# Performance work log

Measured on AMD Instinct MI355X. Metric: run time of the kernel, lower is better.

## Reference

```python
import jax, jax.numpy as jnp
import numpy as np

N_NODES = 100000
N_EDGES = 1600000
IN_C, HID_C, OUT_C = 128, 128, 64


def setup_inputs() -> dict:
    key = jax.random.key(0)
    ks = jax.random.split(key, 8)
    x = jax.random.normal(ks[0], (N_NODES, IN_C), dtype=jnp.float32)
    edge_index = jax.random.randint(ks[1], (2, N_EDGES), 0, N_NODES, dtype=jnp.int32)
    # Glorot-ish init for GCNConv linear weights, zero bias (PyG default)
    def glorot(k, fan_in, fan_out):
        s = jnp.sqrt(6.0 / (fan_in + fan_out))
        return jax.random.uniform(k, (fan_in, fan_out), dtype=jnp.float32, minval=-s, maxval=s)
    return {
        "x": x,
        "edge_index": edge_index,
        "W1": glorot(ks[2], IN_C, HID_C), "b1": jnp.zeros((HID_C,), jnp.float32),
        "W2": glorot(ks[3], HID_C, HID_C), "b2": jnp.zeros((HID_C,), jnp.float32),
        "W3": glorot(ks[4], HID_C, OUT_C), "b3": jnp.zeros((OUT_C,), jnp.float32),
    }


def _gcn_norm(edge_index, num_nodes):
    # Add self-loops (PyG GCNConv default) and compute symmetric normalization
    loops = jnp.arange(num_nodes, dtype=edge_index.dtype)
    src = jnp.concatenate([edge_index[0], loops])  # [E+N]
    dst = jnp.concatenate([edge_index[1], loops])
    deg = jax.ops.segment_sum(jnp.ones_like(dst, dtype=jnp.float32), dst,
                              num_segments=num_nodes)
    deg_inv_sqrt = jnp.where(deg > 0, jax.lax.rsqrt(jnp.maximum(deg, 1.0)), 0.0)
    norm = deg_inv_sqrt[src] * deg_inv_sqrt[dst]  # [E+N]
    return src, dst, norm


def _gcn_layer(x, src, dst, norm, W, b, num_nodes):
    h = x @ W                                # [N, out] dense transform first
    msg = h[src] * norm[:, None]             # gather + scale  [E+N, out]
    out = jax.ops.segment_sum(msg, dst, num_segments=num_nodes)  # scatter-add
    return out + b


def reference(x, edge_index, W1, b1, W2, b2, W3, b3):
    n = x.shape[0]
    src, dst, norm = _gcn_norm(edge_index, n)
    h = jax.nn.relu(_gcn_layer(x, src, dst, norm, W1, b1, n))
    h = jax.nn.relu(_gcn_layer(h, src, dst, norm, W2, b2, n))
    return _gcn_layer(h, src, dst, norm, W3, b3, n)
```

## Files before the change

### kernel.cpp

```cpp
#include <hip/hip_runtime.h>

#define NN 100000
#define NE 1600000
#define NBK 391
#define BSH 8
#define MPAD 100096
#define SCB 391
#define CAP 5120
#define NB64 1563

typedef unsigned short ushortT;
typedef unsigned long long ull;
using sh8 = __attribute__((ext_vector_type(8))) short;
using f4  = __attribute__((ext_vector_type(4))) float;


__device__ __forceinline__ unsigned short bfr(float f) {
  unsigned u = __float_as_uint(f);
  u += 0x7FFF + ((u >> 16) & 1);
  return (unsigned short)(u >> 16);
}
__device__ __forceinline__ float bf2f(unsigned short h) {
  return __uint_as_float(((unsigned)h) << 16);
}
__device__ __forceinline__ void acc8(const uint4 v, float* a) {
  a[0] += __uint_as_float(v.x << 16);
  a[1] += __uint_as_float(v.x & 0xFFFF0000u);
  a[2] += __uint_as_float(v.y << 16);
  a[3] += __uint_as_float(v.y & 0xFFFF0000u);
  a[4] += __uint_as_float(v.z << 16);
  a[5] += __uint_as_float(v.z & 0xFFFF0000u);
  a[6] += __uint_as_float(v.w << 16);
  a[7] += __uint_as_float(v.w & 0xFFFF0000u);
}
__device__ __forceinline__ sh8 hi8(const float4 a, const float4 b) {
  sh8 r;
  r[0] = (short)bfr(a.x); r[1] = (short)bfr(a.y);
  r[2] = (short)bfr(a.z); r[3] = (short)bfr(a.w);
  r[4] = (short)bfr(b.x); r[5] = (short)bfr(b.y);
  r[6] = (short)bfr(b.z); r[7] = (short)bfr(b.w);
  return r;
}


template <int COUT>
__device__ __forceinline__ void packone(const float* __restrict__ W,
                                        ushortT* __restrict__ Bp, int i) {
  const int j = i & 7;
  const int l = (i >> 3) & 63;
  const int rest = i >> 9;
  const int g = rest % (COUT / 16);
  const int ks = rest / (COUT / 16);
  const int k = (ks & 3) * 32 + (l >> 4) * 8 + j;
  const int n = g * 16 + (l & 15);
  const float v = W[k * COUT + n];
  const unsigned short h = bfr(v);
  Bp[i] = (ks < 4) ? h : bfr(v - bf2f(h));
}


__global__ __launch_bounds__(256) void k_scatterpack(
    const int* __restrict__ src, const int* __restrict__ dst,
    int* __restrict__ cursor, unsigned* __restrict__ pairArr,
    const float* __restrict__ W1, const float* __restrict__ W2,
    const float* __restrict__ W3, ushortT* __restrict__ Bp1,
    ushortT* __restrict__ Bp2, ushortT* __restrict__ Bp3) {
  if (blockIdx.x >= SCB) {
    const int i = (blockIdx.x - SCB) * 256 + threadIdx.x;
    if (i < 32768) packone<128>(W1, Bp1, i);
    else if (i < 65536) packone<128>(W2, Bp2, i - 32768);
    else packone<64>(W3, Bp3, i - 65536);
    return;
  }
  __shared__ int lcnt[512];
  __shared__ int lbase[512];
  __shared__ int lrank[NBK];
  __shared__ int bbase[NBK];
  __shared__ int sd2[256];
  __shared__ unsigned sorted[4096];
  __shared__ int target[4096];
  const int t = threadIdx.x;
  for (int i = t; i < 512; i += 256) lcnt[i] = 0;
  for (int i = t; i < NBK; i += 256) lrank[i] = 0;
  __syncthreads();
  const int base = blockIdx.x * 4096;
  int rs[16], rd[16];
#pragma unroll
  for (int q = 0; q < 16; q++) {
    int e = base + t + 256 * q;
    rs[q] = (e < NE) ? src[e] : -1;
    rd[q] = (e < NE) ? dst[e] : -1;
    if (rd[q] >= 0) atomicAdd(&lcnt[rd[q] >> BSH], 1);
  }
  __syncthreads();
  const int s0 = lcnt[2 * t];
  const int s1 = lcnt[2 * t + 1];
  sd2[t] = s0 + s1;
  __syncthreads();
  for (int off = 1; off < 256; off <<= 1) {
    int x = (t >= off) ? sd2[t - off] : 0;
    __syncthreads();
    sd2[t] += x;
    __syncthreads();
  }
  const int epair = sd2[t] - (s0 + s1);
  lbase[2 * t] = epair;
  lbase[2 * t + 1] = epair + s0;
  __syncthreads();
  for (int i = t; i < NBK; i += 256)
    if (lcnt[i] > 0) bbase[i] = atomicAdd(&cursor[i], lcnt[i]);
  __syncthreads();
#pragma unroll
  for (int q = 0; q < 16; q++) {
    if (rd[q] >= 0) {
      int b = rd[q] >> BSH;
      int r = atomicAdd(&lrank[b], 1);
      int slot = lbase[b] + r;
      sorted[slot] = ((unsigned)rs[q] << 8) | ((unsigned)rd[q] & 255u);
      target[slot] = b * CAP + bbase[b] + r;
    }
  }
  __syncthreads();
  const int n = min(4096, NE - base);
  for (int s = t; s < n; s += 256) pairArr[target[s]] = sorted[s];
}


__global__ __launch_bounds__(256) void k_buildcsr(const unsigned* __restrict__ pairArr,
                                                  const int* __restrict__ cnt,
                                                  float* __restrict__ dinv,
                                                  int* __restrict__ rowptr,
                                                  int* __restrict__ col) {
  __shared__ int lc[256];
  __shared__ int sd[256];
  __shared__ int bc[NBK];
  const int t = threadIdx.x;
  const int b = blockIdx.x;
  const int n0 = b << BSH;
  for (int i = t; i < NBK; i += 256) bc[i] = cnt[i];
  lc[t] = 0;
  __syncthreads();
  int partial = 0;
  for (int i = t; i < b; i += 256) partial += bc[i];
  sd[t] = partial;
  __syncthreads();
  for (int off = 128; off > 0; off >>= 1) {
    if (t < off) sd[t] += sd[t + off];
    __syncthreads();
  }
  const int ebeg = sd[0];
  const int myCnt = bc[b];
  __syncthreads();
  const unsigned* pb = pairArr + (size_t)b * CAP;
  for (int i = t; i < myCnt; i += 256)
    atomicAdd(&lc[pb[i] & 255u], 1);
  __syncthreads();
  const int v = lc[t];
  sd[t] = v;
  __syncthreads();
  for (int off = 1; off < 256; off <<= 1) {
    int x = (t >= off) ? sd[t - off] : 0;
    __syncthreads();
    sd[t] += x;
    __syncthreads();
  }
  const int excl = sd[t] - v;
  lc[t] = excl;
  const int node = n0 + t;
  if (node < NN) {
    rowptr[node] = ebeg + excl;
    dinv[node] = rsqrtf(1.0f + (float)v);
  }
  if (b == 0 && t == 0) rowptr[NN] = NE;
  __syncthreads();
  for (int i = t; i < myCnt; i += 256) {
    unsigned p = pb[i];
    int d = (int)(p & 255u);
    int srcv = (int)(p >> 8);
    int pos = atomicAdd(&lc[d], 1);
    col[ebeg + pos] = srcv;
  }
}


template <int COUT, bool FUSED>
__global__ __launch_bounds__(256) void k_gemmM(const ushortT* __restrict__ A,
                                               const float* __restrict__ X,
                                               const ushortT* __restrict__ Bp,
                                               const float* __restrict__ dinv,
                                               ushortT* __restrict__ hs) {
  constexpr int CGALL = COUT / 16;
  constexpr int RG = 2;
  constexpr int CG = 4;
  const int w = threadIdx.x >> 6;
  const int lane = threadIdx.x & 63;
  const int q = lane >> 4;
  const int c = lane & 15;
  int row0, cg0;
  if (COUT == 128) {
    row0 = blockIdx.x * 64 + (w & 1) * 32;
    cg0 = (w >> 1) * 4;
  } else {
    row0 = blockIdx.x * 128 + w * 32;
    cg0 = 0;
  }

  const ushortT* ap[RG];
  const float* xp[RG];
#pragma unroll
  for (int rg = 0; rg < RG; rg++) {
    const int row = row0 + rg * 16 + c;
    if (FUSED) xp[rg] = X + (size_t)min(row, NN - 1) * 128 + q * 8;
    else ap[rg] = A + (size_t)row * 128 + q * 8;
  }
  const ushortT* bp0 = Bp + (size_t)lane * 8;

  f4 acc[RG][CG];
#pragma unroll
  for (int i = 0; i < RG; i++)
#pragma unroll
    for (int j = 0; j < CG; j++) acc[i][j] = (f4){0.f, 0.f, 0.f, 0.f};

  sh8 ah[RG], bh[CG], bl[CG];
  sh8 nah[RG], nbh[CG], nbl[CG];

  auto loadA = [&](int kr, sh8 (&h)[RG]) {
#pragma unroll
    for (int rg = 0; rg < RG; rg++) {
      if (FUSED) {
        const float4 x0 = *reinterpret_cast<const float4*>(xp[rg] + kr * 32);
        const float4 x1 = *reinterpret_cast<const float4*>(xp[rg] + kr * 32 + 4);
        h[rg] = hi8(x0, x1);
      } else {
        h[rg] = *reinterpret_cast<const sh8*>(ap[rg] + kr * 32);
      }
    }
  };
  auto loadB = [&](int kr, sh8 (&h)[CG], sh8 (&l)[CG]) {
#pragma unroll
    for (int cg = 0; cg < CG; cg++) {
      h[cg] = *reinterpret_cast<const sh8*>(bp0 + (size_t)(kr * CGALL + cg0 + cg) * 512);
      l[cg] = *reinterpret_cast<const sh8*>(bp0 + (size_t)((4 + kr) * CGALL + cg0 + cg) * 512);
    }
  };

  loadA(0, ah);
  loadB(0, bh, bl);
#pragma unroll
  for (int kr = 0; kr < 4; kr++) {
    if (kr < 3) {
      loadA(kr + 1, nah);
      loadB(kr + 1, nbh, nbl);
    }
#pragma unroll
    for (int rg = 0; rg < RG; rg++)
#pragma unroll
      for (int cg = 0; cg < CG; cg++)
        acc[rg][cg] = __builtin_amdgcn_mfma_f32_16x16x32_bf16(ah[rg], bh[cg],
                                                              acc[rg][cg], 0, 0, 0);
#pragma unroll
    for (int rg = 0; rg < RG; rg++)
#pragma unroll
      for (int cg = 0; cg < CG; cg++)
        acc[rg][cg] = __builtin_amdgcn_mfma_f32_16x16x32_bf16(ah[rg], bl[cg],
                                                              acc[rg][cg], 0, 0, 0);
    if (kr < 3) {
#pragma unroll
      for (int rg = 0; rg < RG; rg++) ah[rg] = nah[rg];
#pragma unroll
      for (int cg = 0; cg < CG; cg++) { bh[cg] = nbh[cg]; bl[cg] = nbl[cg]; }
    }
  }

#pragma unroll
  for (int rg = 0; rg < RG; rg++) {
#pragma unroll
    for (int reg = 0; reg < 4; reg++) {
      const int row = row0 + rg * 16 + q * 4 + reg;
      if (row < NN) {
        const float dv = dinv[row];
#pragma unroll
        for (int cg = 0; cg < CG; cg++) {
          hs[(size_t)row * COUT + (cg0 + cg) * 16 + c] = bfr(acc[rg][cg][reg] * dv);
        }
      }
    }
  }
}


template <int COUT>
__global__ __launch_bounds__(256) void k_aggemm(
    const ushortT* __restrict__ hs_in, const int* __restrict__ rowptr,
    const int* __restrict__ col, const float* __restrict__ dinv,
    const float* __restrict__ bias, const ushortT* __restrict__ Bp,
    ushortT* __restrict__ hs_out) {
  constexpr int CGALL = COUT / 16;
  __shared__ ushortT At[64 * 128];
  const int t = threadIdx.x;
  const int w = t >> 6;
  const int lane = t & 63;
  const int q = lane >> 4;
  const int c = lane & 15;
  const int chb = c * 8;
  const int n0 = blockIdx.x * 64;

  for (int it = 0; it < 16; ++it) {
    const int r = w * 16 + it;
    const int node = n0 + r;
    float a[8] = {};
    if (node < NN) {
      const int beg = rowptr[node];
      const int end = rowptr[node + 1];
      if (q == 0) {
        const uint4 v = *reinterpret_cast<const uint4*>(hs_in + (long)node * 128 + chb);
        acc8(v, a);
      }
      int j = beg;
      if (j + 8 <= end) {
        int c0 = col[j + q];
        int c1 = col[j + 4 + q];
        while (true) {
          const uint4 v0 = *reinterpret_cast<const uint4*>(hs_in + (long)c0 * 128 + chb);
          const uint4 v1 = *reinterpret_cast<const uint4*>(hs_in + (long)c1 * 128 + chb);
          j += 8;
          const bool more = (j + 8 <= end);
          int m0, m1;
          if (more) { m0 = col[j + q]; m1 = col[j + 4 + q]; }
          acc8(v0, a);
          acc8(v1, a);
          if (!more) break;
          c0 = m0; c1 = m1;
        }
      }
      if (j + 4 <= end) {
        int cc = col[j + q];
        const uint4 v = *reinterpret_cast<const uint4*>(hs_in + (long)cc * 128 + chb);
        acc8(v, a);
        j += 4;
      }
      {
        const int rem = end - j;
        if (q < rem) {
          int cc = col[j + q];
          const uint4 v = *reinterpret_cast<const uint4*>(hs_in + (long)cc * 128 + chb);
          acc8(v, a);
        }
      }
    }
#pragma unroll
    for (int i = 0; i < 8; i++) a[i] += __shfl(a[i], lane ^ 32);
#pragma unroll
    for (int i = 0; i < 8; i++) a[i] += __shfl(a[i], lane ^ 16);
    if (q == 0 && node < NN) {
      const float di = dinv[node];
      const float4 b0 = *reinterpret_cast<const float4*>(bias + chb);
      const float4 b1 = *reinterpret_cast<const float4*>(bias + chb + 4);
      float o[8];
      o[0] = fmaf(a[0], di, b0.x); o[1] = fmaf(a[1], di, b0.y);
      o[2] = fmaf(a[2], di, b0.z); o[3] = fmaf(a[3], di, b0.w);
      o[4] = fmaf(a[4], di, b1.x); o[5] = fmaf(a[5], di, b1.y);
      o[6] = fmaf(a[6], di, b1.z); o[7] = fmaf(a[7], di, b1.w);
#pragma unroll
      for (int i = 0; i < 8; i++) o[i] = fmaxf(o[i], 0.f);
      uint4 H;
      H.x = (unsigned)bfr(o[0]) | ((unsigned)bfr(o[1]) << 16);
      H.y = (unsigned)bfr(o[2]) | ((unsigned)bfr(o[3]) << 16);
      H.z = (unsigned)bfr(o[4]) | ((unsigned)bfr(o[5]) << 16);
      H.w = (unsigned)bfr(o[6]) | ((unsigned)bfr(o[7]) << 16);
      const unsigned bo = (unsigned)(r * 256 + c * 16) ^ (unsigned)((r & 7) << 4);
      *reinterpret_cast<uint4*>(reinterpret_cast<char*>(At) + bo) = H;
    }
  }
  __syncthreads();

  f4 acc[CGALL];
#pragma unroll
  for (int cg = 0; cg < CGALL; ++cg) acc[cg] = (f4){0.f, 0.f, 0.f, 0.f};
  const ushortT* bp0 = Bp + (size_t)lane * 8;
  const int arow = w * 16 + c;
  const char* ab = reinterpret_cast<const char*>(At);
#pragma unroll
  for (int kr = 0; kr < 4; ++kr) {
    const unsigned bo =
        (unsigned)(arow * 256 + kr * 64 + q * 16) ^ (unsigned)((arow & 7) << 4);
    const sh8 af = *reinterpret_cast<const sh8*>(ab + bo);
    sh8 bh[CGALL];
#pragma unroll
    for (int cg = 0; cg < CGALL; ++cg)
      bh[cg] = *reinterpret_cast<const sh8*>(bp0 + (size_t)(kr * CGALL + cg) * 512);
#pragma unroll
    for (int cg = 0; cg < CGALL; ++cg)
      acc[cg] = __builtin_amdgcn_mfma_f32_16x16x32_bf16(af, bh[cg], acc[cg], 0, 0, 0);
#pragma unroll
    for (int cg = 0; cg < CGALL; ++cg)
      bh[cg] = *reinterpret_cast<const sh8*>(bp0 + (size_t)((4 + kr) * CGALL + cg) * 512);
#pragma unroll
    for (int cg = 0; cg < CGALL; ++cg)
      acc[cg] = __builtin_amdgcn_mfma_f32_16x16x32_bf16(af, bh[cg], acc[cg], 0, 0, 0);
  }
#pragma unroll
  for (int reg = 0; reg < 4; ++reg) {
    const int row = n0 + w * 16 + q * 4 + reg;
    if (row < NN) {
      const float dv = dinv[row];
#pragma unroll
      for (int cg = 0; cg < CGALL; ++cg)
        hs_out[(size_t)row * COUT + cg * 16 + c] = bfr(acc[cg][reg] * dv);
    }
  }
}


__global__ __launch_bounds__(256) void k_agg64(const ushortT* __restrict__ hs,
                                               const int* __restrict__ rowptr,
                                               const int* __restrict__ col,
                                               const float* __restrict__ dinv,
                                               const float* __restrict__ bias,
                                               float* __restrict__ out) {
  const int gid = blockIdx.x * 256 + threadIdx.x;
  const int node = gid >> 6;
  if (node >= NN) return;
  const int lane = threadIdx.x & 63;
  const int o8 = lane >> 3;
  const int chb = (lane & 7) * 8;
  const int beg = rowptr[node];
  const int end = rowptr[node + 1];

  float a[8] = {};
  if (o8 == 0) {
    const uint4 v = *reinterpret_cast<const uint4*>(hs + (long)node * 64 + chb);
    acc8(v, a);
  }

  int j = beg;
  if (j + 16 <= end) {
    int c0 = col[j + o8];
    int c1 = col[j + 8 + o8];
    while (true) {
      const uint4 v0 = *reinterpret_cast<const uint4*>(hs + (long)c0 * 64 + chb);
      const uint4 v1 = *reinterpret_cast<const uint4*>(hs + (long)c1 * 64 + chb);
      j += 16;
      const bool more = (j + 16 <= end);
      int n0, n1;
      if (more) { n0 = col[j + o8]; n1 = col[j + 8 + o8]; }
      acc8(v0, a);
      acc8(v1, a);
      if (!more) break;
      c0 = n0; c1 = n1;
    }
  }
  for (; j + 8 <= end; j += 8) {
    int c = col[j + o8];
    const uint4 v = *reinterpret_cast<const uint4*>(hs + (long)c * 64 + chb);
    acc8(v, a);
  }
  {
    const int r = end - j;
    if (o8 < r) {
      int c = col[j + o8];
      const uint4 v = *reinterpret_cast<const uint4*>(hs + (long)c * 64 + chb);
      acc8(v, a);
    }
  }

#pragma unroll
  for (int i = 0; i < 8; i++) a[i] += __shfl(a[i], lane ^ 32);
#pragma unroll
  for (int i = 0; i < 8; i++) a[i] += __shfl(a[i], lane ^ 16);
#pragma unroll
  for (int i = 0; i < 8; i++) a[i] += __shfl(a[i], lane ^ 8);

  if (o8 == 0) {
    const float di = dinv[node];
    const float4 b0 = *reinterpret_cast<const float4*>(bias + chb);
    const float4 b1 = *reinterpret_cast<const float4*>(bias + chb + 4);
    float4 r0, r1;
    r0.x = fmaf(a[0], di, b0.x); r0.y = fmaf(a[1], di, b0.y);
    r0.z = fmaf(a[2], di, b0.z); r0.w = fmaf(a[3], di, b0.w);
    r1.x = fmaf(a[4], di, b1.x); r1.y = fmaf(a[5], di, b1.y);
    r1.z = fmaf(a[6], di, b1.z); r1.w = fmaf(a[7], di, b1.w);
    *reinterpret_cast<float4*>(out + (long)node * 64 + chb) = r0;
    *reinterpret_cast<float4*>(out + (long)node * 64 + chb + 4) = r1;
  }
}


extern "C" void kernel_launch(void* const* d_in, const int* in_sizes, int n_in,
                              void* d_out, int out_size, void* d_ws, size_t ws_size,
                              hipStream_t stream) {
  const float* x  = (const float*)d_in[0];
  const int* ei   = (const int*)d_in[1];
  const float* W1 = (const float*)d_in[2];
  const float* b1 = (const float*)d_in[3];
  const float* W2 = (const float*)d_in[4];
  const float* b2 = (const float*)d_in[5];
  const float* W3 = (const float*)d_in[6];
  const float* b3 = (const float*)d_in[7];
  float* out = (float*)d_out;
  const int* srcp = ei;
  const int* dstp = ei + NE;

  char* wsb = (char*)d_ws;
  size_t off = 0;
  auto alloc = [&](size_t bytes) -> void* {
    void* p = wsb + off;
    off += (bytes + 255) & ~(size_t)255;
    return p;
  };
  ushortT* hs1 = (ushortT*)alloc((size_t)MPAD * 128 * 2);
  ushortT* hs2 = (ushortT*)alloc((size_t)NN * 128 * 2);
  int*   col    = (int*)alloc((size_t)NE * 4);
  int*   rowptr = (int*)alloc((size_t)(NN + 1) * 4);
  float* dinv   = (float*)alloc((size_t)NN * 4);
  int*   cursor = (int*)alloc((size_t)NBK * 4);
  ushortT* Bp1 = (ushortT*)alloc((size_t)32768 * 2);
  ushortT* Bp2 = (ushortT*)alloc((size_t)32768 * 2);
  ushortT* Bp3 = (ushortT*)alloc((size_t)16384 * 2);
  unsigned* pairArr = (unsigned*)hs2;
  ushortT* hs3 = hs1;
  (void)ws_size; (void)in_sizes; (void)n_in; (void)out_size;

  hipMemsetAsync(cursor, 0, (size_t)NBK * 4, stream);
  k_scatterpack<<<SCB + 320, 256, 0, stream>>>(srcp, dstp, cursor, pairArr,
                                               W1, W2, W3, Bp1, Bp2, Bp3);
  k_buildcsr<<<NBK, 256, 0, stream>>>(pairArr, cursor, dinv, rowptr, col);

  const int aggGrid = (NN * 64) / 256;
  const int gemmGrid128 = MPAD / 64;

  k_gemmM<128, true><<<gemmGrid128, 256, 0, stream>>>(nullptr, x, Bp1, dinv, hs1);
  k_aggemm<128><<<NB64, 256, 0, stream>>>(hs1, rowptr, col, dinv, b1, Bp2, hs2);
  k_aggemm<64><<<NB64, 256, 0, stream>>>(hs2, rowptr, col, dinv, b2, Bp3, hs3);
  k_agg64<<<aggGrid, 256, 0, stream>>>(hs3, rowptr, col, dinv, b3, out);
}
```

Before: 386.7 us.

## Use 16 waves per block in fused aggregate-GEMM, splitting nodes and MFMA tiles

The fused aggregate+GEMM kernel now launches 1024 threads per block instead of 256. Each of the 16 waves aggregates 4 nodes instead of 16, and the MFMA stage splits row and column tiles across the waves. rowptr, dinv and bias are loaded once per wave and broadcast with shuffles instead of being reloaded per node. The goal is more waves in flight to hide gather latency in the aggregation. The cost is heavier per-block synchronisation and tighter register limits from the new launch bounds.

```diff
diff --git a/kernel.cpp b/kernel.cpp
--- a/kernel.cpp
+++ b/kernel.cpp
@@ -290,12 +290,13 @@
 
 
 template <int COUT>
-__global__ __launch_bounds__(256) void k_aggemm(
+__global__ __launch_bounds__(1024, 8) void k_aggemm(
     const ushortT* __restrict__ hs_in, const int* __restrict__ rowptr,
     const int* __restrict__ col, const float* __restrict__ dinv,
     const float* __restrict__ bias, const ushortT* __restrict__ Bp,
     ushortT* __restrict__ hs_out) {
   constexpr int CGALL = COUT / 16;
+  constexpr int UPW = (4 * CGALL) / 16;
   __shared__ ushortT At[64 * 128];
   const int t = threadIdx.x;
   const int w = t >> 6;
@@ -304,48 +305,53 @@
   const int c = lane & 15;
   const int chb = c * 8;
   const int n0 = blockIdx.x * 64;
-
-  for (int it = 0; it < 16; ++it) {
-    const int r = w * 16 + it;
-    const int node = n0 + r;
+  const int nw0 = n0 + w * 4;
+
+  const int rpv = rowptr[min(nw0 + (lane & 7), NN)];
+  const float dvv = dinv[min(nw0 + (lane & 3), NN - 1)];
+  const float4 b0 = *reinterpret_cast<const float4*>(bias + chb);
+  const float4 b1 = *reinterpret_cast<const float4*>(bias + chb + 4);
+
+  for (int it = 0; it < 4; ++it) {
+    const int node = nw0 + it;
+    const int r = w * 4 + it;
+    const int beg = __shfl(rpv, it);
+    const int end = __shfl(rpv, it + 1);
+    const float di = __shfl(dvv, it);
     float a[8] = {};
-    if (node < NN) {
-      const int beg = rowptr[node];
-      const int end = rowptr[node + 1];
-      if (q == 0) {
-        const uint4 v = *reinterpret_cast<const uint4*>(hs_in + (long)node * 128 + chb);
-        acc8(v, a);
+    if (node < NN && q == 0) {
+      const uint4 v = *reinterpret_cast<const uint4*>(hs_in + (long)node * 128 + chb);
+      acc8(v, a);
+    }
+    int j = beg;
+    if (j + 8 <= end) {
+      int c0 = col[j + q];
+      int c1 = col[j + 4 + q];
+      while (true) {
+        const uint4 v0 = *reinterpret_cast<const uint4*>(hs_in + (long)c0 * 128 + chb);
+        const uint4 v1 = *reinterpret_cast<const uint4*>(hs_in + (long)c1 * 128 + chb);
+        j += 8;
+        const bool more = (j + 8 <= end);
+        int m0, m1;
+        if (more) { m0 = col[j + q]; m1 = col[j + 4 + q]; }
+        acc8(v0, a);
+        acc8(v1, a);
+        if (!more) break;
+        c0 = m0; c1 = m1;
       }
-      int j = beg;
-      if (j + 8 <= end) {
-        int c0 = col[j + q];
-        int c1 = col[j + 4 + q];
-        while (true) {
-          const uint4 v0 = *reinterpret_cast<const uint4*>(hs_in + (long)c0 * 128 + chb);
-          const uint4 v1 = *reinterpret_cast<const uint4*>(hs_in + (long)c1 * 128 + chb);
-          j += 8;
-          const bool more = (j + 8 <= end);
-          int m0, m1;
-          if (more) { m0 = col[j + q]; m1 = col[j + 4 + q]; }
-          acc8(v0, a);
-          acc8(v1, a);
-          if (!more) break;
-          c0 = m0; c1 = m1;
-        }
-      }
-      if (j + 4 <= end) {
+    }
+    if (j + 4 <= end) {
+      int cc = col[j + q];
+      const uint4 v = *reinterpret_cast<const uint4*>(hs_in + (long)cc * 128 + chb);
+      acc8(v, a);
+      j += 4;
+    }
+    {
+      const int rem = end - j;
+      if (q < rem) {
         int cc = col[j + q];
         const uint4 v = *reinterpret_cast<const uint4*>(hs_in + (long)cc * 128 + chb);
         acc8(v, a);
-        j += 4;
-      }
-      {
-        const int rem = end - j;
-        if (q < rem) {
-          int cc = col[j + q];
-          const uint4 v = *reinterpret_cast<const uint4*>(hs_in + (long)cc * 128 + chb);
-          acc8(v, a);
-        }
       }
     }
 #pragma unroll
@@ -353,9 +359,6 @@
 #pragma unroll
     for (int i = 0; i < 8; i++) a[i] += __shfl(a[i], lane ^ 16);
     if (q == 0 && node < NN) {
-      const float di = dinv[node];
-      const float4 b0 = *reinterpret_cast<const float4*>(bias + chb);
-      const float4 b1 = *reinterpret_cast<const float4*>(bias + chb + 4);
       float o[8];
       o[0] = fmaf(a[0], di, b0.x); o[1] = fmaf(a[1], di, b0.y);
       o[2] = fmaf(a[2], di, b0.z); o[3] = fmaf(a[3], di, b0.w);
@@ -374,39 +377,41 @@
   }
   __syncthreads();
 
-  f4 acc[CGALL];
-#pragma unroll
-  for (int cg = 0; cg < CGALL; ++cg) acc[cg] = (f4){0.f, 0.f, 0.f, 0.f};
+  const int rg = (w * UPW) / CGALL;
+  const int cg0 = (w * UPW) % CGALL;
   const ushortT* bp0 = Bp + (size_t)lane * 8;
-  const int arow = w * 16 + c;
   const char* ab = reinterpret_cast<const char*>(At);
+  const int arow = rg * 16 + c;
+  f4 acc[UPW];
+#pragma unroll
+  for (int u = 0; u < UPW; ++u) acc[u] = (f4){0.f, 0.f, 0.f, 0.f};
 #pragma unroll
   for (int kr = 0; kr < 4; ++kr) {
     const unsigned bo =
         (unsigned)(arow * 256 + kr * 64 + q * 16) ^ (unsigned)((arow & 7) << 4);
     const sh8 af = *reinterpret_cast<const sh8*>(ab + bo);
-    sh8 bh[CGALL];
-#pragma unroll
-    for (int cg = 0; cg < CGALL; ++cg)
-      bh[cg] = *reinterpret_cast<const sh8*>(bp0 + (size_t)(kr * CGALL + cg) * 512);
-#pragma unroll
-    for (int cg = 0; cg < CGALL; ++cg)
-      acc[cg] = __builtin_amdgcn_mfma_f32_16x16x32_bf16(af, bh[cg], acc[cg], 0, 0, 0);
-#pragma unroll
-    for (int cg = 0; cg < CGALL; ++cg)
-      bh[cg] = *reinterpret_cast<const sh8*>(bp0 + (size_t)((4 + kr) * CGALL + cg) * 512);
-#pragma unroll
-    for (int cg = 0; cg < CGALL; ++cg)
-      acc[cg] = __builtin_amdgcn_mfma_f32_16x16x32_bf16(af, bh[cg], acc[cg], 0, 0, 0);
-  }
-#pragma unroll
-  for (int reg = 0; reg < 4; ++reg) {
-    const int row = n0 + w * 16 + q * 4 + reg;
-    if (row < NN) {
-      const float dv = dinv[row];
-#pragma unroll
-      for (int cg = 0; cg < CGALL; ++cg)
-        hs_out[(size_t)row * COUT + cg * 16 + c] = bfr(acc[cg][reg] * dv);
+#pragma unroll
+    for (int u = 0; u < UPW; ++u) {
+      const sh8 bh = *reinterpret_cast<const sh8*>(
+          bp0 + (size_t)(kr * CGALL + cg0 + u) * 512);
+      acc[u] = __builtin_amdgcn_mfma_f32_16x16x32_bf16(af, bh, acc[u], 0, 0, 0);
+    }
+#pragma unroll
+    for (int u = 0; u < UPW; ++u) {
+      const sh8 bl = *reinterpret_cast<const sh8*>(
+          bp0 + (size_t)((4 + kr) * CGALL + cg0 + u) * 512);
+      acc[u] = __builtin_amdgcn_mfma_f32_16x16x32_bf16(af, bl, acc[u], 0, 0, 0);
+    }
+  }
+#pragma unroll
+  for (int u = 0; u < UPW; ++u) {
+#pragma unroll
+    for (int reg = 0; reg < 4; ++reg) {
+      const int row = n0 + rg * 16 + q * 4 + reg;
+      if (row < NN) {
+        hs_out[(size_t)row * COUT + (cg0 + u) * 16 + c] =
+            bfr(acc[u][reg] * dinv[row]);
+      }
     }
   }
 }
@@ -530,7 +535,7 @@
   const int gemmGrid128 = MPAD / 64;
 
   k_gemmM<128, true><<<gemmGrid128, 256, 0, stream>>>(nullptr, x, Bp1, dinv, hs1);
-  k_aggemm<128><<<NB64, 256, 0, stream>>>(hs1, rowptr, col, dinv, b1, Bp2, hs2);
-  k_aggemm<64><<<NB64, 256, 0, stream>>>(hs2, rowptr, col, dinv, b2, Bp3, hs3);
+  k_aggemm<128><<<NB64, 1024, 0, stream>>>(hs1, rowptr, col, dinv, b1, Bp2, hs2);
+  k_aggemm<64><<<NB64, 1024, 0, stream>>>(hs2, rowptr, col, dinv, b2, Bp3, hs3);
   k_agg64<<<aggGrid, 256, 0, stream>>>(hs3, rowptr, col, dinv, b3, out);
 }
```

After: 370.1 us. -4.3%, faster.
